# Performance work log

Measured on AMD Instinct MI355X. Metric: run time of the kernel, lower is better.

The kernel has to match this reference:

```python
import jax, jax.numpy as jnp
import numpy as np

ALPHA = 1.0

def _soft_assign(x, clusters, alpha=ALPHA):
    # (avoids materializing the (N, K, D) broadcast intermediate)
    x_sq = jnp.sum(x * x, axis=1, keepdims=True)            # (N, 1)
    c_sq = jnp.sum(clusters * clusters, axis=1)             # (K,)
    cross = jnp.einsum('nd,kd->nk', x, clusters)            # (N, K)
    dist_sq = jnp.maximum(x_sq + c_sq[None, :] - 2.0 * cross, 0.0)
    q = 1.0 / (1.0 + dist_sq / alpha)
    q = q ** ((alpha + 1.0) / 2.0)
    return q / jnp.sum(q, axis=1, keepdims=True)            # row-normalize

def setup_inputs() -> dict:
    key = jax.random.key(0)
    k1, k2 = jax.random.split(key)
    N, D, K = 65536, 512, 1024
    x = jax.random.normal(k1, (N, D), dtype=jnp.float32)
    # xavier_uniform for (K, D): limit = sqrt(6 / (K + D))
    limit = float(np.sqrt(6.0 / (K + D)))
    clusters = jax.random.uniform(k2, (K, D), dtype=jnp.float32, minval=-limit, maxval=limit)
    return {"x": x, "clusters": clusters}

def reference(x, clusters):
    return _soft_assign(x, clusters)
```

## Files before the change

kernel.cpp:

```cpp
#include <hip/hip_runtime.h>

typedef __bf16 bf16x8 __attribute__((ext_vector_type(8)));
typedef float f32x16 __attribute__((ext_vector_type(16)));
typedef unsigned short ushort8 __attribute__((ext_vector_type(8)));

__device__ __forceinline__ unsigned short f2bf(float f) {
    unsigned int u = __float_as_uint(f);
    u += 0x7FFFu + ((u >> 16) & 1u);
    return (unsigned short)(u >> 16);
}


__global__ __launch_bounds__(256) void prep_all(
    const float* __restrict__ x, const float* __restrict__ cl,
    unsigned short* __restrict__ xbf, unsigned short* __restrict__ cbf,
    float* __restrict__ csq, float* __restrict__ xsq) {
    const int bid = blockIdx.x;
    const int t   = threadIdx.x;
    if (bid < 4096) {
        const int gx  = bid * 256 + t;
        const int row = gx >> 4, c = gx & 15;
        const float4* xg = (const float4*)(x + ((size_t)row << 9) + c * 32);
        float4 v[8];
#pragma unroll
        for (int i = 0; i < 8; ++i) v[i] = xg[i];
        float ssq = 0.f;
#pragma unroll
        for (int i = 0; i < 8; ++i)
            ssq += v[i].x*v[i].x + v[i].y*v[i].y + v[i].z*v[i].z + v[i].w*v[i].w;
#pragma unroll
        for (int off = 1; off <= 8; off <<= 1) ssq += __shfl_xor(ssq, off);
        if ((t & 15) == 0) xsq[row] = ssq;

        const int rb = row >> 6, mt = (row >> 5) & 1, n = row & 31;
#pragma unroll
        for (int g = 0; g < 4; ++g) {
            const float4 a = v[2*g], b = v[2*g+1];
            ushort8 h;
            h[0]=f2bf(a.x); h[1]=f2bf(a.y); h[2]=f2bf(a.z); h[3]=f2bf(a.w);
            h[4]=f2bf(b.x); h[5]=f2bf(b.y); h[6]=f2bf(b.z); h[7]=f2bf(b.w);
            const int d0 = c * 32 + g * 8;
            const int sl = d0 >> 4, kh = (d0 >> 3) & 1;
            *(ushort8*)(xbf + (size_t)rb * 32768 +
                        (size_t)(((mt * 32 + sl) * 64 + kh * 32 + n)) * 8) = h;
        }
    } else {
        const int row  = (bid - 4096) * 4 + (t >> 6);
        const int lane = t & 63;
        const float4* cg = (const float4*)(cl + ((size_t)row << 9) + lane * 8);
        float4 v0 = cg[0], v1 = cg[1];
        float ssq = v0.x*v0.x + v0.y*v0.y + v0.z*v0.z + v0.w*v0.w
                  + v1.x*v1.x + v1.y*v1.y + v1.z*v1.z + v1.w*v1.w;
        ushort8 h;
        h[0]=f2bf(v0.x); h[1]=f2bf(v0.y); h[2]=f2bf(v0.z); h[3]=f2bf(v0.w);
        h[4]=f2bf(v1.x); h[5]=f2bf(v1.y); h[6]=f2bf(v1.z); h[7]=f2bf(v1.w);
        const int n = row & 31, T = row >> 5;
        const int s = lane >> 1, hh = lane & 1;
        *(ushort8*)(cbf + (size_t)((T * 32 + s) * 64 + hh * 32 + n) * 8) = h;
#pragma unroll
        for (int off = 32; off >= 1; off >>= 1) ssq += __shfl_xor(ssq, off);
        if (lane == 0) csq[row] = ssq;
    }
}

__device__ __forceinline__ void stage_a(const unsigned short* __restrict__ src,
                                        unsigned short* dst) {
#pragma unroll
    for (int i = 0; i < 4; ++i)
        __builtin_amdgcn_global_load_lds(
            (const __attribute__((address_space(1))) unsigned int*)(src + i * 512),
            (__attribute__((address_space(3))) unsigned int*)(dst + i * 512),
            16, 0, 0);
}

__global__ __launch_bounds__(1024, 4) void soft_assign2(
    const unsigned short* __restrict__ xbf, const unsigned short* __restrict__ cbf,
    const float* __restrict__ csq, const float* __restrict__ xsq,
    float* __restrict__ out) {
    __shared__ unsigned short xs[2][32768];
    __shared__ float part[64 * 32];
    __shared__ float xsql[2][64];
    __shared__ float inv[64];

    const int t    = threadIdx.x;
    const int lane = t & 63;
    const int w    = t >> 6;
    const int l31  = lane & 31;
    const int half = lane >> 5;

    part[t] = 0.f;
    part[t + 1024] = 0.f;

    const int col0   = w * 64 + l31;
    const float csq0 = csq[col0];
    const float csq1 = csq[col0 + 32];

    const unsigned short* bT0 = cbf + ((size_t)(2 * w) * 2048 + lane) * 8;
    const unsigned short* bT1 = bT0 + 16384;

    stage_a(xbf + (size_t)blockIdx.x * 32768 + (w * 4) * 512 + lane * 8,
            &xs[0][(w * 4) * 512]);
    if (t < 64) xsql[0][t] = xsq[blockIdx.x * 64 + t];
    asm volatile("s_waitcnt vmcnt(0)" ::: "memory");
    __syncthreads();

    int buf = 0;
#pragma unroll 1
    for (int ri = 0; ri < 4; ++ri) {
        const int rb = blockIdx.x + 256 * ri;
        const unsigned short* aB = &xs[buf][0] + lane * 8;

        f32x16 c00, c01, c10, c11;
#pragma unroll
        for (int i = 0; i < 16; ++i) { c00[i]=0.f; c01[i]=0.f; c10[i]=0.f; c11[i]=0.f; }

        bf16x8 b0c = *(const bf16x8*)(bT0);
        bf16x8 b1c = *(const bf16x8*)(bT1);
        bf16x8 b0n = *(const bf16x8*)(bT0 + 512);
        bf16x8 b1n = *(const bf16x8*)(bT1 + 512);

#pragma unroll 4
        for (int sl = 0; sl < 32; sl += 2) {
            const int sp2 = (sl + 2) & 31;
            const int sp3 = (sl + 3) & 31;
            bf16x8 p0 = *(const bf16x8*)(bT0 + sp2 * 512);
            bf16x8 p1 = *(const bf16x8*)(bT1 + sp2 * 512);
            bf16x8 q0 = *(const bf16x8*)(bT0 + sp3 * 512);
            bf16x8 q1 = *(const bf16x8*)(bT1 + sp3 * 512);
            bf16x8 a0 = *(const bf16x8*)(aB + sl * 512);
            bf16x8 a1 = *(const bf16x8*)(aB + 16384 + sl * 512);
            bf16x8 a2 = *(const bf16x8*)(aB + (sl + 1) * 512);
            bf16x8 a3 = *(const bf16x8*)(aB + 16384 + (sl + 1) * 512);
            __builtin_amdgcn_s_setprio(1);
            c00 = __builtin_amdgcn_mfma_f32_32x32x16_bf16(a0, b0c, c00, 0, 0, 0);
            c01 = __builtin_amdgcn_mfma_f32_32x32x16_bf16(a0, b1c, c01, 0, 0, 0);
            c10 = __builtin_amdgcn_mfma_f32_32x32x16_bf16(a1, b0c, c10, 0, 0, 0);
            c11 = __builtin_amdgcn_mfma_f32_32x32x16_bf16(a1, b1c, c11, 0, 0, 0);
            c00 = __builtin_amdgcn_mfma_f32_32x32x16_bf16(a2, b0n, c00, 0, 0, 0);
            c01 = __builtin_amdgcn_mfma_f32_32x32x16_bf16(a2, b1n, c01, 0, 0, 0);
            c10 = __builtin_amdgcn_mfma_f32_32x32x16_bf16(a3, b0n, c10, 0, 0, 0);
            c11 = __builtin_amdgcn_mfma_f32_32x32x16_bf16(a3, b1n, c11, 0, 0, 0);
            __builtin_amdgcn_s_setprio(0);
            b0c = p0; b1c = p1; b0n = q0; b1n = q1;
        }

        if (ri < 3) {
            stage_a(xbf + (size_t)(rb + 256) * 32768 + (w * 4) * 512 + lane * 8,
                    &xs[buf ^ 1][(w * 4) * 512]);
            if (t < 64) xsql[buf ^ 1][t] = xsq[(rb + 256) * 64 + t];
        }

        const float* xq = xsql[buf];
#pragma unroll
        for (int r = 0; r < 16; ++r) {
            const int rl0 = (r & 3) + 8 * (r >> 2) + 4 * half;
            const float x0 = xq[rl0];
            const float x1 = xq[rl0 + 32];
            float q00 = __builtin_amdgcn_rcpf(1.f + fmaxf(x0 + csq0 - 2.f * c00[r], 0.f));
            float q01 = __builtin_amdgcn_rcpf(1.f + fmaxf(x0 + csq1 - 2.f * c01[r], 0.f));
            float q10 = __builtin_amdgcn_rcpf(1.f + fmaxf(x1 + csq0 - 2.f * c10[r], 0.f));
            float q11 = __builtin_amdgcn_rcpf(1.f + fmaxf(x1 + csq1 - 2.f * c11[r], 0.f));
            c00[r] = q00; c01[r] = q01; c10[r] = q10; c11[r] = q11;
            atomicAdd(&part[rl0 * 32 + l31], q00 + q01);
            atomicAdd(&part[(rl0 + 32) * 32 + l31], q10 + q11);
        }
        __syncthreads();
        if (t < 64) {
            float s = 0.f;
#pragma unroll
            for (int c2 = 0; c2 < 32; ++c2) {
                const int idx = t * 32 + ((c2 + t) & 31);
                s += part[idx];
                part[idx] = 0.f;
            }
            inv[t] = __builtin_amdgcn_rcpf(s);
        }
        asm volatile("s_waitcnt vmcnt(0)" ::: "memory");
        __syncthreads();

        float* og = out + (size_t)rb * 65536;
#pragma unroll
        for (int r = 0; r < 16; ++r) {
            const int rl0 = (r & 3) + 8 * (r >> 2) + 4 * half;
            const float i0 = inv[rl0];
            const float i1 = inv[rl0 + 32];
            og[(size_t)rl0 * 1024 + col0]             = c00[r] * i0;
            og[(size_t)rl0 * 1024 + col0 + 32]        = c01[r] * i0;
            og[(size_t)(rl0 + 32) * 1024 + col0]      = c10[r] * i1;
            og[(size_t)(rl0 + 32) * 1024 + col0 + 32] = c11[r] * i1;
        }
        buf ^= 1;
    }
}


__global__ __launch_bounds__(256) void prep_clusters(
    const float* __restrict__ cl, unsigned short* __restrict__ cbf,
    float* __restrict__ csq) {
    const int row  = blockIdx.x * 4 + (threadIdx.x >> 6);
    const int lane = threadIdx.x & 63;
    const float4* cg = (const float4*)(cl + ((size_t)row << 9) + lane * 8);
    float4 v0 = cg[0], v1 = cg[1];
    float ssq = v0.x*v0.x + v0.y*v0.y + v0.z*v0.z + v0.w*v0.w
              + v1.x*v1.x + v1.y*v1.y + v1.z*v1.z + v1.w*v1.w;
    ushort8 h;
    h[0]=f2bf(v0.x); h[1]=f2bf(v0.y); h[2]=f2bf(v0.z); h[3]=f2bf(v0.w);
    h[4]=f2bf(v1.x); h[5]=f2bf(v1.y); h[6]=f2bf(v1.z); h[7]=f2bf(v1.w);
    const int n = row & 31, T = row >> 5;
    const int s = lane >> 1, hh = lane & 1;
    *(ushort8*)(cbf + (size_t)((T * 32 + s) * 64 + hh * 32 + n) * 8) = h;
#pragma unroll
    for (int off = 32; off >= 1; off >>= 1) ssq += __shfl_xor(ssq, off);
    if (lane == 0) csq[row] = ssq;
}

__global__ __launch_bounds__(1024, 4) void soft_assign(
    const float* __restrict__ x, const unsigned short* __restrict__ cbf,
    const float* __restrict__ csq, float* __restrict__ out) {
    __shared__ unsigned short xs[2048 * 8];
    __shared__ float part[64 * 32];
    __shared__ float xsq[64];
    __shared__ float inv[64];

    const int t    = threadIdx.x;
    const int lane = t & 63;
    const int w    = t >> 6;
    const int l31  = lane & 31;
    const int half = lane >> 5;
    const int rb   = blockIdx.x;

    part[t] = 0.f;
    part[t + 1024] = 0.f;
    if (t < 64) xsq[t] = 0.f;

    const int col0   = w * 64 + l31;
    const float csq0 = csq[col0];
    const float csq1 = csq[col0 + 32];

    f32x16 c00, c01, c10, c11;
#pragma unroll
    for (int i = 0; i < 16; ++i) { c00[i] = 0.f; c01[i] = 0.f; c10[i] = 0.f; c11[i] = 0.f; }

    const unsigned short* bT0 = cbf + ((size_t)(2 * w) * 32 * 64 + lane) * 8;
    const unsigned short* bT1 = cbf + ((size_t)(2 * w + 1) * 32 * 64 + lane) * 8;
    const unsigned short* aB  = xs + lane * 8;

    bf16x8 b0c = *(const bf16x8*)(bT0);
    bf16x8 b1c = *(const bf16x8*)(bT1);
    bf16x8 b0n = *(const bf16x8*)(bT0 + 512);
    bf16x8 b1n = *(const bf16x8*)(bT1 + 512);

#pragma unroll 1
    for (int ch = 0; ch < 2; ++ch) {
        if (ch) __syncthreads();
#pragma unroll
        for (int i = 0; i < 2; ++i) {
            const int g  = 2 * t + i;
            const int l  = g & 63;
            const int sl = (g >> 6) & 15;
            const int mt = g >> 10;
            const int row = mt * 32 + (l & 31);
            const int d0  = ch * 256 + sl * 16 + (l >> 5) * 8;
            const float4* xg = (const float4*)(x + (size_t)(rb * 64 + row) * 512 + d0);
            float4 v0 = xg[0], v1 = xg[1];
            ushort8 h;
            h[0]=f2bf(v0.x); h[1]=f2bf(v0.y); h[2]=f2bf(v0.z); h[3]=f2bf(v0.w);
            h[4]=f2bf(v1.x); h[5]=f2bf(v1.y); h[6]=f2bf(v1.z); h[7]=f2bf(v1.w);
            *(ushort8*)(xs + (size_t)g * 8) = h;
            float ss = v0.x*v0.x + v0.y*v0.y + v0.z*v0.z + v0.w*v0.w
                     + v1.x*v1.x + v1.y*v1.y + v1.z*v1.z + v1.w*v1.w;
            atomicAdd(&xsq[row], ss);
        }
        __syncthreads();

#pragma unroll 1
        for (int sl = 0; sl < 16; sl += 2) {
            const int sg  = ch * 16 + sl;
            const int sp2 = (sg + 2) & 31;
            const int sp3 = (sg + 3) & 31;
            bf16x8 p0 = *(const bf16x8*)(bT0 + sp2 * 512);
            bf16x8 p1 = *(const bf16x8*)(bT1 + sp2 * 512);
            bf16x8 q0 = *(const bf16x8*)(bT0 + sp3 * 512);
            bf16x8 q1 = *(const bf16x8*)(bT1 + sp3 * 512);
            bf16x8 a0 = *(const bf16x8*)(aB + (sl)     * 512);
            bf16x8 a1 = *(const bf16x8*)(aB + 8192 + (sl)     * 512);
            bf16x8 a2 = *(const bf16x8*)(aB + (sl + 1) * 512);
            bf16x8 a3 = *(const bf16x8*)(aB + 8192 + (sl + 1) * 512);
            c00 = __builtin_amdgcn_mfma_f32_32x32x16_bf16(a0, b0c, c00, 0, 0, 0);
            c01 = __builtin_amdgcn_mfma_f32_32x32x16_bf16(a0, b1c, c01, 0, 0, 0);
            c10 = __builtin_amdgcn_mfma_f32_32x32x16_bf16(a1, b0c, c10, 0, 0, 0);
            c11 = __builtin_amdgcn_mfma_f32_32x32x16_bf16(a1, b1c, c11, 0, 0, 0);
            c00 = __builtin_amdgcn_mfma_f32_32x32x16_bf16(a2, b0n, c00, 0, 0, 0);
            c01 = __builtin_amdgcn_mfma_f32_32x32x16_bf16(a2, b1n, c01, 0, 0, 0);
            c10 = __builtin_amdgcn_mfma_f32_32x32x16_bf16(a3, b0n, c10, 0, 0, 0);
            c11 = __builtin_amdgcn_mfma_f32_32x32x16_bf16(a3, b1n, c11, 0, 0, 0);
            b0c = p0; b1c = p1; b0n = q0; b1n = q1;
        }
    }

#pragma unroll
    for (int r = 0; r < 16; ++r) {
        const int rl0 = (r & 3) + 8 * (r >> 2) + 4 * half;
        const float x0 = xsq[rl0];
        const float x1 = xsq[rl0 + 32];
        float q00 = __builtin_amdgcn_rcpf(1.f + fmaxf(x0 + csq0 - 2.f * c00[r], 0.f));
        float q01 = __builtin_amdgcn_rcpf(1.f + fmaxf(x0 + csq1 - 2.f * c01[r], 0.f));
        float q10 = __builtin_amdgcn_rcpf(1.f + fmaxf(x1 + csq0 - 2.f * c10[r], 0.f));
        float q11 = __builtin_amdgcn_rcpf(1.f + fmaxf(x1 + csq1 - 2.f * c11[r], 0.f));
        c00[r] = q00; c01[r] = q01; c10[r] = q10; c11[r] = q11;
        atomicAdd(&part[rl0 * 32 + l31], q00 + q01);
        atomicAdd(&part[(rl0 + 32) * 32 + l31], q10 + q11);
    }
    __syncthreads();
    if (t < 64) {
        float s = 0.f;
#pragma unroll
        for (int c = 0; c < 32; ++c) s += part[t * 32 + ((c + t) & 31)];
        inv[t] = __builtin_amdgcn_rcpf(s);
    }
    __syncthreads();

    float* og = out + (size_t)rb * 64 * 1024;
#pragma unroll
    for (int r = 0; r < 16; ++r) {
        const int rl0 = (r & 3) + 8 * (r >> 2) + 4 * half;
        const float i0 = inv[rl0];
        const float i1 = inv[rl0 + 32];
        og[(size_t)rl0 * 1024 + col0]             = c00[r] * i0;
        og[(size_t)rl0 * 1024 + col0 + 32]        = c01[r] * i0;
        og[(size_t)(rl0 + 32) * 1024 + col0]      = c10[r] * i1;
        og[(size_t)(rl0 + 32) * 1024 + col0 + 32] = c11[r] * i1;
    }
}

extern "C" void kernel_launch(void* const* d_in, const int* in_sizes, int n_in,
                              void* d_out, int out_size, void* d_ws, size_t ws_size,
                              hipStream_t stream) {
    const float* x  = (const float*)d_in[0];
    const float* cl = (const float*)d_in[1];
    float* out = (float*)d_out;

    const size_t CBF_OFF = 0;
    const size_t CSQ_OFF = 1048576;
    const size_t XSQ_OFF = 1052672;
    const size_t XBF_OFF = 1314816;
    const size_t NEED    = 68423680;

    if (ws_size >= NEED) {
        unsigned short* cbf = (unsigned short*)((char*)d_ws + CBF_OFF);
        float*          csq = (float*)((char*)d_ws + CSQ_OFF);
        float*          xsq = (float*)((char*)d_ws + XSQ_OFF);
        unsigned short* xbf = (unsigned short*)((char*)d_ws + XBF_OFF);
        prep_all<<<4352, 256, 0, stream>>>(x, cl, xbf, cbf, csq, xsq);
        soft_assign2<<<256, 1024, 0, stream>>>(xbf, cbf, csq, xsq, out);
    } else {
        unsigned short* cbf = (unsigned short*)d_ws;
        float* csq = (float*)((char*)d_ws + (size_t)1024 * 512 * 2);
        prep_clusters<<<256, 256, 0, stream>>>(cl, cbf, csq);
        soft_assign<<<1024, 1024, 0, stream>>>(x, cbf, csq, out);
    }
}
```

Baseline: 645.7 us.

## Stream cluster operand through LDS ring and single-buffer the x tile

The cluster B operand used to be loaded straight from global memory into registers. Each wave now pulls it through its own LDS ring with global_load_lds, using a two-stage software pipeline and vmcnt waits. The x tile drops from double to single buffering, so the next tile is only staged after the MFMA loop and a barrier, which gives up overlap of the A prefetch with compute. Output stores become nontemporal, and extra barriers and a vmcnt wait are added at the end of each row block.

```diff
diff --git a/kernel.cpp b/kernel.cpp
--- a/kernel.cpp
+++ b/kernel.cpp
@@ -73,13 +73,22 @@
             16, 0, 0);
 }
 
-__global__ __launch_bounds__(1024, 4) void soft_assign2(
+__device__ __forceinline__ void gload1(const unsigned short* __restrict__ src,
+                                       unsigned short* dst) {
+    __builtin_amdgcn_global_load_lds(
+        (const __attribute__((address_space(1))) unsigned int*)(src),
+        (__attribute__((address_space(3))) unsigned int*)(dst),
+        16, 0, 0);
+}
+
+__global__ __launch_bounds__(1024, 4) void soft_assign3(
     const unsigned short* __restrict__ xbf, const unsigned short* __restrict__ cbf,
     const float* __restrict__ csq, const float* __restrict__ xsq,
     float* __restrict__ out) {
-    __shared__ unsigned short xs[2][32768];
+    __shared__ unsigned short xs[32768];
+    __shared__ unsigned short bring[32768];
     __shared__ float part[64 * 32];
-    __shared__ float xsql[2][64];
+    __shared__ float xsql[64];
     __shared__ float inv[64];
 
     const int t    = threadIdx.x;
@@ -95,67 +104,74 @@
     const float csq0 = csq[col0];
     const float csq1 = csq[col0 + 32];
 
-    const unsigned short* bT0 = cbf + ((size_t)(2 * w) * 2048 + lane) * 8;
-    const unsigned short* bT1 = bT0 + 16384;
+    const unsigned short* bsrc0 = cbf + (size_t)(2 * w) * 16384 + lane * 8;
+    const unsigned short* bsrc1 = bsrc0 + 16384;
+    unsigned short* brw = bring + w * 2048;
+    const unsigned short* brl = brw + lane * 8;
+    const unsigned short* aB  = xs + lane * 8;
 
     stage_a(xbf + (size_t)blockIdx.x * 32768 + (w * 4) * 512 + lane * 8,
-            &xs[0][(w * 4) * 512]);
-    if (t < 64) xsql[0][t] = xsq[blockIdx.x * 64 + t];
+            xs + (w * 4) * 512);
     asm volatile("s_waitcnt vmcnt(0)" ::: "memory");
     __syncthreads();
 
-    int buf = 0;
 #pragma unroll 1
     for (int ri = 0; ri < 4; ++ri) {
         const int rb = blockIdx.x + 256 * ri;
-        const unsigned short* aB = &xs[buf][0] + lane * 8;
+
+        if (t < 64) xsql[t] = xsq[rb * 64 + t];
 
         f32x16 c00, c01, c10, c11;
 #pragma unroll
         for (int i = 0; i < 16; ++i) { c00[i]=0.f; c01[i]=0.f; c10[i]=0.f; c11[i]=0.f; }
 
-        bf16x8 b0c = *(const bf16x8*)(bT0);
-        bf16x8 b1c = *(const bf16x8*)(bT1);
-        bf16x8 b0n = *(const bf16x8*)(bT0 + 512);
-        bf16x8 b1n = *(const bf16x8*)(bT1 + 512);
-
-#pragma unroll 4
-        for (int sl = 0; sl < 32; sl += 2) {
-            const int sp2 = (sl + 2) & 31;
-            const int sp3 = (sl + 3) & 31;
-            bf16x8 p0 = *(const bf16x8*)(bT0 + sp2 * 512);
-            bf16x8 p1 = *(const bf16x8*)(bT1 + sp2 * 512);
-            bf16x8 q0 = *(const bf16x8*)(bT0 + sp3 * 512);
-            bf16x8 q1 = *(const bf16x8*)(bT1 + sp3 * 512);
-            bf16x8 a0 = *(const bf16x8*)(aB + sl * 512);
-            bf16x8 a1 = *(const bf16x8*)(aB + 16384 + sl * 512);
-            bf16x8 a2 = *(const bf16x8*)(aB + (sl + 1) * 512);
-            bf16x8 a3 = *(const bf16x8*)(aB + 16384 + (sl + 1) * 512);
+        gload1(bsrc0,       brw);
+        gload1(bsrc1,       brw + 512);
+        gload1(bsrc0 + 512, brw + 1024);
+        gload1(bsrc1 + 512, brw + 1536);
+        asm volatile("s_waitcnt vmcnt(2)" ::: "memory");
+        bf16x8 bc0 = *(const bf16x8*)(brl);
+        bf16x8 bc1 = *(const bf16x8*)(brl + 512);
+        bf16x8 ac0 = *(const bf16x8*)(aB);
+        bf16x8 ac1 = *(const bf16x8*)(aB + 16384);
+
+#pragma unroll
+        for (int s = 0; s < 32; ++s) {
+            if (s < 30) {
+                gload1(bsrc0 + (s + 2) * 512, brw + ((s & 1) * 2 + 0) * 512);
+                gload1(bsrc1 + (s + 2) * 512, brw + ((s & 1) * 2 + 1) * 512);
+                asm volatile("s_waitcnt vmcnt(2)" ::: "memory");
+            } else if (s == 30) {
+                asm volatile("s_waitcnt vmcnt(0)" ::: "memory");
+            }
+            bf16x8 bn0, bn1, an0, an1;
+            if (s < 31) {
+                const int sn = (s + 1) & 1;
+                bn0 = *(const bf16x8*)(brl + (sn * 2 + 0) * 512);
+                bn1 = *(const bf16x8*)(brl + (sn * 2 + 1) * 512);
+                an0 = *(const bf16x8*)(aB + (s + 1) * 512);
+                an1 = *(const bf16x8*)(aB + 16384 + (s + 1) * 512);
+            }
             __builtin_amdgcn_s_setprio(1);
-            c00 = __builtin_amdgcn_mfma_f32_32x32x16_bf16(a0, b0c, c00, 0, 0, 0);
-            c01 = __builtin_amdgcn_mfma_f32_32x32x16_bf16(a0, b1c, c01, 0, 0, 0);
-            c10 = __builtin_amdgcn_mfma_f32_32x32x16_bf16(a1, b0c, c10, 0, 0, 0);
-            c11 = __builtin_amdgcn_mfma_f32_32x32x16_bf16(a1, b1c, c11, 0, 0, 0);
-            c00 = __builtin_amdgcn_mfma_f32_32x32x16_bf16(a2, b0n, c00, 0, 0, 0);
-            c01 = __builtin_amdgcn_mfma_f32_32x32x16_bf16(a2, b1n, c01, 0, 0, 0);
-            c10 = __builtin_amdgcn_mfma_f32_32x32x16_bf16(a3, b0n, c10, 0, 0, 0);
-            c11 = __builtin_amdgcn_mfma_f32_32x32x16_bf16(a3, b1n, c11, 0, 0, 0);
+            c00 = __builtin_amdgcn_mfma_f32_32x32x16_bf16(ac0, bc0, c00, 0, 0, 0);
+            c01 = __builtin_amdgcn_mfma_f32_32x32x16_bf16(ac0, bc1, c01, 0, 0, 0);
+            c10 = __builtin_amdgcn_mfma_f32_32x32x16_bf16(ac1, bc0, c10, 0, 0, 0);
+            c11 = __builtin_amdgcn_mfma_f32_32x32x16_bf16(ac1, bc1, c11, 0, 0, 0);
             __builtin_amdgcn_s_setprio(0);
-            b0c = p0; b1c = p1; b0n = q0; b1n = q1;
-        }
-
-        if (ri < 3) {
+            if (s < 31) { ac0 = an0; ac1 = an1; bc0 = bn0; bc1 = bn1; }
+        }
+
+        __syncthreads();
+
+        if (ri < 3)
             stage_a(xbf + (size_t)(rb + 256) * 32768 + (w * 4) * 512 + lane * 8,
-                    &xs[buf ^ 1][(w * 4) * 512]);
-            if (t < 64) xsql[buf ^ 1][t] = xsq[(rb + 256) * 64 + t];
-        }
-
-        const float* xq = xsql[buf];
+                    xs + (w * 4) * 512);
+
 #pragma unroll
         for (int r = 0; r < 16; ++r) {
             const int rl0 = (r & 3) + 8 * (r >> 2) + 4 * half;
-            const float x0 = xq[rl0];
-            const float x1 = xq[rl0 + 32];
+            const float x0 = xsql[rl0];
+            const float x1 = xsql[rl0 + 32];
             float q00 = __builtin_amdgcn_rcpf(1.f + fmaxf(x0 + csq0 - 2.f * c00[r], 0.f));
             float q01 = __builtin_amdgcn_rcpf(1.f + fmaxf(x0 + csq1 - 2.f * c01[r], 0.f));
             float q10 = __builtin_amdgcn_rcpf(1.f + fmaxf(x1 + csq0 - 2.f * c10[r], 0.f));
@@ -175,7 +191,6 @@
             }
             inv[t] = __builtin_amdgcn_rcpf(s);
         }
-        asm volatile("s_waitcnt vmcnt(0)" ::: "memory");
         __syncthreads();
 
         float* og = out + (size_t)rb * 65536;
@@ -184,12 +199,13 @@
             const int rl0 = (r & 3) + 8 * (r >> 2) + 4 * half;
             const float i0 = inv[rl0];
             const float i1 = inv[rl0 + 32];
-            og[(size_t)rl0 * 1024 + col0]             = c00[r] * i0;
-            og[(size_t)rl0 * 1024 + col0 + 32]        = c01[r] * i0;
-            og[(size_t)(rl0 + 32) * 1024 + col0]      = c10[r] * i1;
-            og[(size_t)(rl0 + 32) * 1024 + col0 + 32] = c11[r] * i1;
-        }
-        buf ^= 1;
+            __builtin_nontemporal_store(c00[r] * i0, &og[(size_t)rl0 * 1024 + col0]);
+            __builtin_nontemporal_store(c01[r] * i0, &og[(size_t)rl0 * 1024 + col0 + 32]);
+            __builtin_nontemporal_store(c10[r] * i1, &og[(size_t)(rl0 + 32) * 1024 + col0]);
+            __builtin_nontemporal_store(c11[r] * i1, &og[(size_t)(rl0 + 32) * 1024 + col0 + 32]);
+        }
+        asm volatile("s_waitcnt vmcnt(0)" ::: "memory");
+        __syncthreads();
     }
 }
 
@@ -352,7 +368,7 @@
         float*          xsq = (float*)((char*)d_ws + XSQ_OFF);
         unsigned short* xbf = (unsigned short*)((char*)d_ws + XBF_OFF);
         prep_all<<<4352, 256, 0, stream>>>(x, cl, xbf, cbf, csq, xsq);
-        soft_assign2<<<256, 1024, 0, stream>>>(xbf, cbf, csq, xsq, out);
+        soft_assign3<<<256, 1024, 0, stream>>>(xbf, cbf, csq, xsq, out);
     } else {
         unsigned short* cbf = (unsigned short*)d_ws;
         float* csq = (float*)((char*)d_ws + (size_t)1024 * 512 * 2);
```

New measurement: 778.7 us. +20.6%, slower.
